# Kernel optimization log

Measured on AMD Instinct MI355X. Metric: run time of the kernel, lower is better.

The kernel has to match this reference:

```python
import jax, jax.numpy as jnp
import numpy as np

MODES_X = 16
MODES_Y = 16


def setup_inputs() -> dict:
    key = jax.random.key(0)
    ks = jax.random.split(key, 8)
    B, H, W, C = 32, 128, 128, 64
    scale = 1.0 / (C * C)
    x = jax.random.normal(ks[0], (B, H, W, C), dtype=jnp.float32)
    w1_real = scale * jax.random.normal(ks[1], (MODES_X, MODES_Y, C, C), dtype=jnp.float32)
    w1_imag = scale * jax.random.normal(ks[2], (MODES_X, MODES_Y, C, C), dtype=jnp.float32)
    w2_real = scale * jax.random.normal(ks[3], (MODES_X, MODES_Y, C, C), dtype=jnp.float32)
    w2_imag = scale * jax.random.normal(ks[4], (MODES_X, MODES_Y, C, C), dtype=jnp.float32)
    dense_kernel = jax.random.normal(ks[5], (C, C), dtype=jnp.float32) / np.sqrt(C)
    dense_bias = jnp.zeros((C,), dtype=jnp.float32)
    return {"x": x, "w1_real": w1_real, "w1_imag": w1_imag,
            "w2_real": w2_real, "w2_imag": w2_imag,
            "dense_kernel": dense_kernel, "dense_bias": dense_bias}


def _spectral_conv2d(x, w1, w2, mx, my):
    # x: [B,H,W,C] real; w1,w2: [mx,my,C,C] complex
    B, H, W, C = x.shape
    x_ft = jnp.fft.rfft2(x, axes=(1, 2))  # [B,H,W//2+1,C] complex64
    out_ft = jnp.zeros((B, H, W // 2 + 1, C), dtype=x_ft.dtype)
    # low positive x-frequencies
    out_ft = out_ft.at[:, :mx, :my].set(
        jnp.einsum('bxyi,xyio->bxyo', x_ft[:, :mx, :my], w1))
    # low negative x-frequencies
    out_ft = out_ft.at[:, -mx:, :my].set(
        jnp.einsum('bxyi,xyio->bxyo', x_ft[:, -mx:, :my], w2))
    return jnp.fft.irfft2(out_ft, s=(H, W), axes=(1, 2))


def reference(x, w1_real, w1_imag, w2_real, w2_imag, dense_kernel, dense_bias):
    w1 = w1_real + 1j * w1_imag
    w2 = w2_real + 1j * w2_imag
    y_s = _spectral_conv2d(x, w1, w2, MODES_X, MODES_Y)
    y_p = jnp.einsum('bhwi,io->bhwo', x, dense_kernel) + dense_bias
    return jax.nn.gelu(x + y_s + y_p, approximate=True)
```

## Files before the change

### kernel.cpp

```cpp
#include <hip/hip_runtime.h>
#include <math.h>

#define BB 32
#define HH 128
#define WW 128
#define CC 64
#define MX 16
#define MY 16
#define NKX 32

#define TWOPI 6.283185307179586f

typedef __attribute__((ext_vector_type(8))) short bf16x8;
typedef __attribute__((ext_vector_type(4))) float f32x4;

__device__ inline unsigned short f2bf(float f) {
    union { float f; unsigned u; } v; v.f = f;
    unsigned r = v.u + 0x7FFFu + ((v.u >> 16) & 1u);
    return (unsigned short)(r >> 16);
}


__global__ __launch_bounds__(256) void kT(const float* __restrict__ K, unsigned short* __restrict__ FR) {
    __shared__ float2 tw[128];
    int tid = threadIdx.x;
    if (tid < 128) {
        float s, c;
        sincosf(TWOPI * (float)tid * (1.0f / 128.0f), &s, &c);
        tw[tid] = make_float2(c, s);
    }
    __syncthreads();
    int g = blockIdx.x * 256 + tid;
    short v[8];
    if (g < 512) {
        int s = g;
        int l = s & 63, ks = (s >> 6) & 3, mt = s >> 8;
        int q = l >> 4, r = l & 15;
        int row = mt * 16 + r, ky = row >> 1, ri = row & 1;
        int k0 = ks * 32 + q * 8;
        #pragma unroll
        for (int e = 0; e < 8; ++e) {
            float2 t = tw[(ky * (k0 + e)) & 127];
            v[e] = (short)f2bf(ri ? -t.y : t.x);
        }
    } else if (g < 2560) {
        int s = g - 512;
        int l = s & 63, ks = (s >> 6) & 7, mt = s >> 9;
        int q = l >> 4, r = l & 15;
        int row = mt * 16 + r, kxi = row >> 1, rr = row & 1;
        int kx = (kxi < 16) ? kxi : (96 + kxi);
        int k0 = ks * 32 + q * 8;
        #pragma unroll
        for (int e = 0; e < 8; ++e) {
            int k = k0 + e, h = k >> 1, ri = k & 1;
            float2 t = tw[(kx * h) & 127];
            float val = (rr == 0) ? (ri == 0 ? t.x : t.y) : (ri == 0 ? -t.y : t.x);
            v[e] = (short)f2bf(val);
        }
    } else if (g < 3584) {
        int s = g - 2560;
        int l = s & 63, ks = (s >> 6) & 1, mt = s >> 7;
        int q = l >> 4, r = l & 15;
        int h = mt * 16 + r;
        int k0 = ks * 32 + q * 8;
        #pragma unroll
        for (int e = 0; e < 8; ++e) {
            int k = k0 + e, kxi = k >> 1, ri = k & 1;
            int kx = (kxi < 16) ? kxi : (96 + kxi);
            float2 t = tw[(kx * h) & 127];
            v[e] = (short)f2bf(ri == 0 ? t.x : -t.y);
        }
    } else if (g < 4096) {
        int s = g - 3584;
        int l = s & 63, tm = s >> 6;
        int q = l >> 4, r = l & 15;
        int row = tm * 16 + r;
        const float inv = 1.0f / 16384.0f;
        #pragma unroll
        for (int e = 0; e < 8; ++e) {
            int ky = 4 * q + (e >> 1);
            float sc = ((ky == 0) ? 1.0f : 2.0f) * inv;
            float2 t = tw[(ky * row) & 127];
            v[e] = (short)f2bf((e & 1) ? (-t.y * sc) : (t.x * sc));
        }
    } else {
        int s = g - 4096;
        int l = s & 63, ks = (s >> 6) & 1, nt = s >> 7;
        int q = l >> 4, r = l & 15;
        int col = nt * 16 + r;
        #pragma unroll
        for (int e = 0; e < 8; ++e) {
            int k = ks * 32 + q * 8 + e;
            v[e] = (short)f2bf(K[k * CC + col]);
        }
    }
    *(bf16x8*)&FR[(size_t)g * 8] = *(const bf16x8*)v;
}

__global__ __launch_bounds__(256) void kA(const float* __restrict__ x, const unsigned short* __restrict__ FR,
                                          unsigned short* __restrict__ X1) {
    int tid = threadIdx.x, bh = blockIdx.x;
    int lane = tid & 63, nt = tid >> 6, q = lane >> 4, r = lane & 15;
    const float* xp = x + (size_t)bh * (WW * CC);
    bf16x8 bf[4];
    #pragma unroll
    for (int ks = 0; ks < 4; ++ks) {
        short v[8];
        #pragma unroll
        for (int e = 0; e < 8; ++e)
            v[e] = (short)f2bf(xp[(ks * 32 + q * 8 + e) * CC + nt * 16 + r]);
        bf[ks] = *(const bf16x8*)v;
    }
    f32x4 acc0 = {0.f, 0.f, 0.f, 0.f}, acc1 = {0.f, 0.f, 0.f, 0.f};
    #pragma unroll
    for (int ks = 0; ks < 4; ++ks) {
        bf16x8 a0 = *(const bf16x8*)&FR[((size_t)((0 * 4 + ks) * 64 + lane)) * 8];
        bf16x8 a1 = *(const bf16x8*)&FR[((size_t)((1 * 4 + ks) * 64 + lane)) * 8];
        acc0 = __builtin_amdgcn_mfma_f32_16x16x32_bf16(a0, bf[ks], acc0, 0, 0, 0);
        acc1 = __builtin_amdgcn_mfma_f32_16x16x32_bf16(a1, bf[ks], acc1, 0, 0, 0);
    }
    int b = bh >> 7, h = bh & 127;
    int c = nt * 16 + r;
    #pragma unroll
    for (int j = 0; j < 4; ++j) {
        int m0 = q * 4 + j;
        X1[(((size_t)b * 16 + (m0 >> 1)) * 128 + h) * 128 + (m0 & 1) * 64 + c] = f2bf(acc0[j]);
        int m1 = 16 + m0;
        X1[(((size_t)b * 16 + (m1 >> 1)) * 128 + h) * 128 + (m1 & 1) * 64 + c] = f2bf(acc1[j]);
    }
}

__global__ __launch_bounds__(256) void kB(const unsigned short* __restrict__ X1, const unsigned short* __restrict__ FR,
                                          unsigned short* __restrict__ X2) {
    int tid = threadIdx.x, blk = blockIdx.x;
    int b = blk >> 4, ky = blk & 15;
    const unsigned short* FB = FR + 4096;
    const unsigned short* p = X1 + ((size_t)b * 16 + ky) * 16384;
    int lane = tid & 63, wid = tid >> 6, q = lane >> 4, r = lane & 15;
    int col = wid * 16 + r;
    bf16x8 bf[8];
    #pragma unroll
    for (int ks = 0; ks < 8; ++ks) {
        short v[8];
        #pragma unroll
        for (int e = 0; e < 8; ++e)
            v[e] = (short)p[(ks * 32 + q * 8 + e) * 64 + col];
        bf[ks] = *(const bf16x8*)v;
    }
    #pragma unroll
    for (int mt = 0; mt < 4; ++mt) {
        f32x4 acc = {0.f, 0.f, 0.f, 0.f};
        #pragma unroll
        for (int ks = 0; ks < 8; ++ks) {
            bf16x8 a = *(const bf16x8*)&FB[((size_t)((mt * 8 + ks) * 64 + lane)) * 8];
            acc = __builtin_amdgcn_mfma_f32_16x16x32_bf16(a, bf[ks], acc, 0, 0, 0);
        }
        #pragma unroll
        for (int j = 0; j < 4; ++j) {
            int m = mt * 16 + q * 4 + j;
            int kxi = m >> 1, rr = m & 1;
            X2[(((size_t)b * NKX + kxi) * 16 + ky) * 128 + 2 * col + rr] = f2bf(acc[j]);
        }
    }
}

__global__ __launch_bounds__(256) void kC(const float* __restrict__ w1r, const float* __restrict__ w1i,
                                          const float* __restrict__ w2r, const float* __restrict__ w2i,
                                          const unsigned short* __restrict__ X2, unsigned short* __restrict__ G) {
    __shared__ float wsr[CC * CC];
    __shared__ float wsi[CC * CC];
    int tid = threadIdx.x;
    int blk = blockIdx.x;
    int kxi = blk >> 4, ky = blk & 15;
    const float* wr = (kxi < 16) ? w1r : w2r;
    const float* wi = (kxi < 16) ? w1i : w2i;
    int wx = (kxi < 16) ? kxi : (kxi - 16);
    size_t woff = ((size_t)wx * MY + ky) * (CC * CC);
    for (int i = tid * 4; i < CC * CC; i += 1024) {
        *(float4*)&wsr[i] = *(const float4*)&wr[woff + i];
        *(float4*)&wsi[i] = *(const float4*)&wi[woff + i];
    }
    __syncthreads();

    int lane = tid & 63, wid = tid >> 6;
    int q = lane >> 4, r = lane & 15;
    bf16x8 af[2][4];
    #pragma unroll
    for (int mt = 0; mt < 2; ++mt) {
        int b = mt * 16 + r;
        #pragma unroll
        for (int ks = 0; ks < 4; ++ks)
            af[mt][ks] = *(const bf16x8*)&X2[(((size_t)b * NKX + kxi) * 16 + ky) * 128 + ks * 32 + q * 8];
    }
    bf16x8 bfr[2][4];
    #pragma unroll
    for (int t = 0; t < 2; ++t) {
        int n = (wid * 2 + t) * 16 + r;
        int o = n >> 1, ro = n & 1;
        #pragma unroll
        for (int ks = 0; ks < 4; ++ks) {
            short v[8];
            #pragma unroll
            for (int e = 0; e < 8; ++e) {
                int k = ks * 32 + q * 8 + e;
                int i = k >> 1, ri = k & 1;
                float val = (ri == 0) ? (ro ? wsi[i * 64 + o] : wsr[i * 64 + o])
                                      : (ro ? wsr[i * 64 + o] : -wsi[i * 64 + o]);
                v[e] = (short)f2bf(val);
            }
            bfr[t][ks] = *(const bf16x8*)v;
        }
    }
    f32x4 acc[2][2] = {{{0.f,0.f,0.f,0.f},{0.f,0.f,0.f,0.f}},{{0.f,0.f,0.f,0.f},{0.f,0.f,0.f,0.f}}};
    #pragma unroll
    for (int ks = 0; ks < 4; ++ks)
        #pragma unroll
        for (int mt = 0; mt < 2; ++mt)
            #pragma unroll
            for (int t = 0; t < 2; ++t)
                acc[mt][t] = __builtin_amdgcn_mfma_f32_16x16x32_bf16(af[mt][ks], bfr[t][ks], acc[mt][t], 0, 0, 0);
    #pragma unroll
    for (int mt = 0; mt < 2; ++mt)
        #pragma unroll
        for (int t = 0; t < 2; ++t)
            #pragma unroll
            for (int j = 0; j < 4; ++j) {
                int b = mt * 16 + q * 4 + j;
                int n = (wid * 2 + t) * 16 + r;
                G[(((size_t)b * NKX + kxi) * 16 + ky) * 128 + n] = f2bf(acc[mt][t][j]);
            }
}

__global__ __launch_bounds__(256) void kD(const unsigned short* __restrict__ G, const unsigned short* __restrict__ FR,
                                          unsigned short* __restrict__ Zf) {
    int tid = threadIdx.x, blk = blockIdx.x;
    int b = blk >> 5, ky = (blk >> 1) & 15, mh = blk & 1;
    int lane = tid & 63, wid = tid >> 6, q = lane >> 4, r = lane & 15;
    const unsigned short* FD = FR + 20480;
    bf16x8 bfr[2][2];
    #pragma unroll
    for (int t = 0; t < 2; ++t) {
        int n = (wid * 2 + t) * 16 + r;
        #pragma unroll
        for (int ks = 0; ks < 2; ++ks) {
            short v[8];
            #pragma unroll
            for (int e = 0; e < 8; ++e) {
                int k = ks * 32 + q * 8 + e;
                int kxi = k >> 1, ri = k & 1;
                unsigned short raw = G[(((size_t)b * NKX + kxi) * 16 + ky) * 128 + (n ^ ri)];
                if (ri & (n & 1)) raw ^= 0x8000u;
                v[e] = (short)raw;
            }
            bfr[t][ks] = *(const bf16x8*)v;
        }
    }
    #pragma unroll
    for (int mt2 = 0; mt2 < 4; ++mt2) {
        int mt = mh * 4 + mt2;
        f32x4 acc[2] = {{0.f,0.f,0.f,0.f},{0.f,0.f,0.f,0.f}};
        #pragma unroll
        for (int ks = 0; ks < 2; ++ks) {
            bf16x8 a = *(const bf16x8*)&FD[((size_t)((mt * 2 + ks) * 64 + lane)) * 8];
            #pragma unroll
            for (int t = 0; t < 2; ++t)
                acc[t] = __builtin_amdgcn_mfma_f32_16x16x32_bf16(a, bfr[t][ks], acc[t], 0, 0, 0);
        }
        #pragma unroll
        for (int t = 0; t < 2; ++t)
            #pragma unroll
            for (int j = 0; j < 4; ++j) {
                int h = mt * 16 + q * 4 + j;
                int n = (wid * 2 + t) * 16 + r;
                int c = n >> 1, reim = n & 1;
                int kp = 2 * ky + reim, q2 = kp >> 3, e2 = kp & 7;
                int nt2 = c >> 4, r2 = c & 15;
                Zf[(((size_t)b * 128 + h) * 4 + nt2) * 512 + (q2 * 16 + r2) * 8 + e2] = f2bf(acc[t][j]);
            }
    }
}

__global__ __launch_bounds__(256) void kE(const float* __restrict__ x, const unsigned short* __restrict__ Zf,
                                          const unsigned short* __restrict__ FR,
                                          const float* __restrict__ bias, float* __restrict__ out) {
    __shared__ float xs[WW * 68];
    int tid = threadIdx.x, bh = blockIdx.x;
    const float* xp = x + (size_t)bh * (WW * CC);
    for (int i = tid * 4; i < WW * CC; i += 1024) {
        int w = i >> 6, c = i & 63;
        *(float4*)&xs[w * 68 + c] = *(const float4*)&xp[i];
    }
    __syncthreads();
    int lane = tid & 63, wv = tid >> 6, q = lane >> 4, r = lane & 15;
    const unsigned short* FEAT = FR + 28672;
    const unsigned short* FEBK = FR + 32768;
    bf16x8 ax[2][2], at[2];
    #pragma unroll
    for (int t2 = 0; t2 < 2; ++t2) {
        int tm = wv * 2 + t2;
        int row = tm * 16 + r;
        #pragma unroll
        for (int ks = 0; ks < 2; ++ks) {
            const float* s = &xs[row * 68 + ks * 32 + q * 8];
            short v[8];
            #pragma unroll
            for (int e = 0; e < 8; ++e) v[e] = (short)f2bf(s[e]);
            ax[t2][ks] = *(const bf16x8*)v;
        }
        at[t2] = *(const bf16x8*)&FEAT[((size_t)(tm * 64 + lane)) * 8];
    }
    #pragma unroll
    for (int nt = 0; nt < 4; ++nt) {
        bf16x8 b0 = *(const bf16x8*)&FEBK[((size_t)((nt * 2 + 0) * 64 + lane)) * 8];
        bf16x8 b1 = *(const bf16x8*)&FEBK[((size_t)((nt * 2 + 1) * 64 + lane)) * 8];
        bf16x8 bz = *(const bf16x8*)&Zf[((size_t)bh * 4 + nt) * 512 + lane * 8];
        int c = nt * 16 + r;
        float bsv = bias[c];
        #pragma unroll
        for (int t2 = 0; t2 < 2; ++t2) {
            int tm = wv * 2 + t2;
            f32x4 acc = {0.f, 0.f, 0.f, 0.f};
            acc = __builtin_amdgcn_mfma_f32_16x16x32_bf16(ax[t2][0], b0, acc, 0, 0, 0);
            acc = __builtin_amdgcn_mfma_f32_16x16x32_bf16(ax[t2][1], b1, acc, 0, 0, 0);
            acc = __builtin_amdgcn_mfma_f32_16x16x32_bf16(at[t2], bz, acc, 0, 0, 0);
            #pragma unroll
            for (int j = 0; j < 4; ++j) {
                int w = tm * 16 + q * 4 + j;
                float u = acc[j] + xs[w * 68 + c] + bsv;
                float t = u + 0.044715f * u * u * u;
                float e = __expf(-1.5957691216057308f * t);
                out[(size_t)bh * (WW * CC) + w * CC + c] = u / (1.0f + e);
            }
        }
    }
}

extern "C" void kernel_launch(void* const* d_in, const int* in_sizes, int n_in,
                              void* d_out, int out_size, void* d_ws, size_t ws_size,
                              hipStream_t stream) {
    const float* x   = (const float*)d_in[0];
    const float* w1r = (const float*)d_in[1];
    const float* w1i = (const float*)d_in[2];
    const float* w2r = (const float*)d_in[3];
    const float* w2i = (const float*)d_in[4];
    const float* dk  = (const float*)d_in[5];
    const float* db  = (const float*)d_in[6];
    float* out = (float*)d_out;

    unsigned short* FR = (unsigned short*)d_ws;
    unsigned short* X1 = FR + 65536;
    unsigned short* X2 = X1 + 8388608;
    unsigned short* G  = X2 + 2097152;
    unsigned short* Zf = G  + 2097152;

    kT<<<18, 256, 0, stream>>>(dk, FR);
    kA<<<BB * HH, 256, 0, stream>>>(x, FR, X1);
    kB<<<BB * MY, 256, 0, stream>>>(X1, FR, X2);
    kC<<<NKX * MY, 256, 0, stream>>>(w1r, w1i, w2r, w2i, X2, G);
    kD<<<BB * MY * 2, 256, 0, stream>>>(G, FR, Zf);
    kE<<<BB * HH, 256, 0, stream>>>(x, Zf, FR, db, out);
}
```

Baseline: 321.2 us.

## Stage global loads and stores through shared memory for coalesced access in kA-kD

Each of kernels kA, kB, kC and kD now loads its input tile into shared memory with vectorized, coalesced reads before building MFMA fragments. Where a kernel scatters its output, it first writes to a shared-memory tile and then stores to global memory in 16-byte vectors. kC also converts the weights to bf16 while staging them, which halves its LDS footprint. The aim is to remove strided, element-wise global accesses, at the cost of extra barriers and more LDS use, which may lower occupancy.

```diff
diff --git a/kernel.cpp b/kernel.cpp
--- a/kernel.cpp
+++ b/kernel.cpp
@@ -99,76 +99,106 @@
 
 __global__ __launch_bounds__(256) void kA(const float* __restrict__ x, const unsigned short* __restrict__ FR,
                                           unsigned short* __restrict__ X1) {
+    __shared__ unsigned short xbf[WW * CC];
     int tid = threadIdx.x, bh = blockIdx.x;
+    const float* xp = x + (size_t)bh * (WW * CC);
+    for (int i = tid * 4; i < WW * CC; i += 1024) {
+        float4 v = *(const float4*)&xp[i];
+        ushort4 pk = make_ushort4(f2bf(v.x), f2bf(v.y), f2bf(v.z), f2bf(v.w));
+        *(ushort4*)&xbf[i] = pk;
+    }
+    __syncthreads();
     int lane = tid & 63, nt = tid >> 6, q = lane >> 4, r = lane & 15;
-    const float* xp = x + (size_t)bh * (WW * CC);
-    bf16x8 bf[4];
+    bf16x8 bfv[4];
     #pragma unroll
     for (int ks = 0; ks < 4; ++ks) {
         short v[8];
         #pragma unroll
         for (int e = 0; e < 8; ++e)
-            v[e] = (short)f2bf(xp[(ks * 32 + q * 8 + e) * CC + nt * 16 + r]);
-        bf[ks] = *(const bf16x8*)v;
+            v[e] = (short)xbf[(ks * 32 + q * 8 + e) * CC + nt * 16 + r];
+        bfv[ks] = *(const bf16x8*)v;
     }
     f32x4 acc0 = {0.f, 0.f, 0.f, 0.f}, acc1 = {0.f, 0.f, 0.f, 0.f};
     #pragma unroll
     for (int ks = 0; ks < 4; ++ks) {
         bf16x8 a0 = *(const bf16x8*)&FR[((size_t)((0 * 4 + ks) * 64 + lane)) * 8];
         bf16x8 a1 = *(const bf16x8*)&FR[((size_t)((1 * 4 + ks) * 64 + lane)) * 8];
-        acc0 = __builtin_amdgcn_mfma_f32_16x16x32_bf16(a0, bf[ks], acc0, 0, 0, 0);
-        acc1 = __builtin_amdgcn_mfma_f32_16x16x32_bf16(a1, bf[ks], acc1, 0, 0, 0);
-    }
-    int b = bh >> 7, h = bh & 127;
+        acc0 = __builtin_amdgcn_mfma_f32_16x16x32_bf16(a0, bfv[ks], acc0, 0, 0, 0);
+        acc1 = __builtin_amdgcn_mfma_f32_16x16x32_bf16(a1, bfv[ks], acc1, 0, 0, 0);
+    }
+    __syncthreads();
+    unsigned short* asT = xbf;
     int c = nt * 16 + r;
     #pragma unroll
     for (int j = 0; j < 4; ++j) {
         int m0 = q * 4 + j;
-        X1[(((size_t)b * 16 + (m0 >> 1)) * 128 + h) * 128 + (m0 & 1) * 64 + c] = f2bf(acc0[j]);
-        int m1 = 16 + m0;
-        X1[(((size_t)b * 16 + (m1 >> 1)) * 128 + h) * 128 + (m1 & 1) * 64 + c] = f2bf(acc1[j]);
-    }
+        asT[m0 * 64 + c] = f2bf(acc0[j]);
+        asT[(16 + m0) * 64 + c] = f2bf(acc1[j]);
+    }
+    __syncthreads();
+    int b = bh >> 7, h = bh & 127;
+    int ky = tid >> 4, idx8 = tid & 15;
+    int ri = idx8 >> 3, c0 = (idx8 & 7) * 8;
+    bf16x8 vv = *(const bf16x8*)&asT[(2 * ky + ri) * 64 + c0];
+    *(bf16x8*)&X1[(((size_t)b * 16 + ky) * 128 + h) * 128 + ri * 64 + c0] = vv;
 }
 
 __global__ __launch_bounds__(256) void kB(const unsigned short* __restrict__ X1, const unsigned short* __restrict__ FR,
                                           unsigned short* __restrict__ X2) {
+    __shared__ unsigned short xb[256 * 64];
     int tid = threadIdx.x, blk = blockIdx.x;
     int b = blk >> 4, ky = blk & 15;
+    const unsigned short* p = X1 + ((size_t)b * 16 + ky) * 16384;
+    for (int i = tid * 8; i < 256 * 64; i += 2048)
+        *(bf16x8*)&xb[i] = *(const bf16x8*)&p[i];
+    __syncthreads();
     const unsigned short* FB = FR + 4096;
-    const unsigned short* p = X1 + ((size_t)b * 16 + ky) * 16384;
     int lane = tid & 63, wid = tid >> 6, q = lane >> 4, r = lane & 15;
     int col = wid * 16 + r;
-    bf16x8 bf[8];
+    bf16x8 bfv[8];
     #pragma unroll
     for (int ks = 0; ks < 8; ++ks) {
         short v[8];
         #pragma unroll
         for (int e = 0; e < 8; ++e)
-            v[e] = (short)p[(ks * 32 + q * 8 + e) * 64 + col];
-        bf[ks] = *(const bf16x8*)v;
-    }
-    #pragma unroll
-    for (int mt = 0; mt < 4; ++mt) {
-        f32x4 acc = {0.f, 0.f, 0.f, 0.f};
-        #pragma unroll
-        for (int ks = 0; ks < 8; ++ks) {
+            v[e] = (short)xb[(ks * 32 + q * 8 + e) * 64 + col];
+        bfv[ks] = *(const bf16x8*)v;
+    }
+    f32x4 acc[4] = {{0.f,0.f,0.f,0.f},{0.f,0.f,0.f,0.f},{0.f,0.f,0.f,0.f},{0.f,0.f,0.f,0.f}};
+    #pragma unroll
+    for (int ks = 0; ks < 8; ++ks) {
+        #pragma unroll
+        for (int mt = 0; mt < 4; ++mt) {
             bf16x8 a = *(const bf16x8*)&FB[((size_t)((mt * 8 + ks) * 64 + lane)) * 8];
-            acc = __builtin_amdgcn_mfma_f32_16x16x32_bf16(a, bf[ks], acc, 0, 0, 0);
-        }
-        #pragma unroll
-        for (int j = 0; j < 4; ++j) {
-            int m = mt * 16 + q * 4 + j;
-            int kxi = m >> 1, rr = m & 1;
-            X2[(((size_t)b * NKX + kxi) * 16 + ky) * 128 + 2 * col + rr] = f2bf(acc[j]);
-        }
-    }
+            acc[mt] = __builtin_amdgcn_mfma_f32_16x16x32_bf16(a, bfv[ks], acc[mt], 0, 0, 0);
+        }
+    }
+    __syncthreads();
+    unsigned short* asT = xb;
+    #pragma unroll
+    for (int mt = 0; mt < 4; ++mt)
+        #pragma unroll
+        for (int j = 0; j < 4; ++j)
+            asT[(mt * 16 + q * 4 + j) * 64 + col] = f2bf(acc[mt][j]);
+    __syncthreads();
+    int kxi = tid >> 3, part = tid & 7;
+    short v2[16];
+    #pragma unroll
+    for (int s = 0; s < 16; ++s) {
+        int n = part * 16 + s, cc2 = n >> 1, rr = n & 1;
+        v2[s] = (short)asT[(2 * kxi + rr) * 64 + cc2];
+    }
+    unsigned short* dst = &X2[(((size_t)b * NKX + kxi) * 16 + ky) * 128 + part * 16];
+    *(bf16x8*)&dst[0] = *(const bf16x8*)&v2[0];
+    *(bf16x8*)&dst[8] = *(const bf16x8*)&v2[8];
 }
 
 __global__ __launch_bounds__(256) void kC(const float* __restrict__ w1r, const float* __restrict__ w1i,
                                           const float* __restrict__ w2r, const float* __restrict__ w2i,
                                           const unsigned short* __restrict__ X2, unsigned short* __restrict__ G) {
-    __shared__ float wsr[CC * CC];
-    __shared__ float wsi[CC * CC];
+    __shared__ unsigned short wbr[CC * CC];
+    __shared__ unsigned short wbi[CC * CC];
+    __shared__ unsigned short asT[32 * 128];
     int tid = threadIdx.x;
     int blk = blockIdx.x;
     int kxi = blk >> 4, ky = blk & 15;
@@ -177,8 +207,10 @@
     int wx = (kxi < 16) ? kxi : (kxi - 16);
     size_t woff = ((size_t)wx * MY + ky) * (CC * CC);
     for (int i = tid * 4; i < CC * CC; i += 1024) {
-        *(float4*)&wsr[i] = *(const float4*)&wr[woff + i];
-        *(float4*)&wsi[i] = *(const float4*)&wi[woff + i];
+        float4 a = *(const float4*)&wr[woff + i];
+        float4 bq = *(const float4*)&wi[woff + i];
+        *(ushort4*)&wbr[i] = make_ushort4(f2bf(a.x), f2bf(a.y), f2bf(a.z), f2bf(a.w));
+        *(ushort4*)&wbi[i] = make_ushort4(f2bf(bq.x), f2bf(bq.y), f2bf(bq.z), f2bf(bq.w));
     }
     __syncthreads();
 
@@ -204,9 +236,9 @@
             for (int e = 0; e < 8; ++e) {
                 int k = ks * 32 + q * 8 + e;
                 int i = k >> 1, ri = k & 1;
-                float val = (ri == 0) ? (ro ? wsi[i * 64 + o] : wsr[i * 64 + o])
-                                      : (ro ? wsr[i * 64 + o] : -wsi[i * 64 + o]);
-                v[e] = (short)f2bf(val);
+                unsigned short raw = (ri == 0) ? (ro ? wbi[i * 64 + o] : wbr[i * 64 + o])
+                                               : (ro ? wbr[i * 64 + o] : (unsigned short)(wbi[i * 64 + o] ^ 0x8000u));
+                v[e] = (short)raw;
             }
             bfr[t][ks] = *(const bf16x8*)v;
         }
@@ -224,17 +256,27 @@
         #pragma unroll
         for (int t = 0; t < 2; ++t)
             #pragma unroll
-            for (int j = 0; j < 4; ++j) {
-                int b = mt * 16 + q * 4 + j;
-                int n = (wid * 2 + t) * 16 + r;
-                G[(((size_t)b * NKX + kxi) * 16 + ky) * 128 + n] = f2bf(acc[mt][t][j]);
-            }
+            for (int j = 0; j < 4; ++j)
+                asT[(mt * 16 + q * 4 + j) * 128 + (wid * 2 + t) * 16 + r] = f2bf(acc[mt][t][j]);
+    __syncthreads();
+    int bb = tid >> 3, part = tid & 7;
+    bf16x8 u0 = *(const bf16x8*)&asT[bb * 128 + part * 16];
+    bf16x8 u1 = *(const bf16x8*)&asT[bb * 128 + part * 16 + 8];
+    unsigned short* dst = &G[(((size_t)bb * NKX + kxi) * 16 + ky) * 128 + part * 16];
+    *(bf16x8*)&dst[0] = u0;
+    *(bf16x8*)&dst[8] = u1;
 }
 
 __global__ __launch_bounds__(256) void kD(const unsigned short* __restrict__ G, const unsigned short* __restrict__ FR,
                                           unsigned short* __restrict__ Zf) {
+    __shared__ unsigned short gs[NKX * 128];
     int tid = threadIdx.x, blk = blockIdx.x;
     int b = blk >> 5, ky = (blk >> 1) & 15, mh = blk & 1;
+    for (int i = tid * 8; i < NKX * 128; i += 2048) {
+        int kxi = i >> 7, n = i & 127;
+        *(bf16x8*)&gs[i] = *(const bf16x8*)&G[(((size_t)b * NKX + kxi) * 16 + ky) * 128 + n];
+    }
+    __syncthreads();
     int lane = tid & 63, wid = tid >> 6, q = lane >> 4, r = lane & 15;
     const unsigned short* FD = FR + 20480;
     bf16x8 bfr[2][2];
@@ -248,7 +290,7 @@
             for (int e = 0; e < 8; ++e) {
                 int k = ks * 32 + q * 8 + e;
                 int kxi = k >> 1, ri = k & 1;
-                unsigned short raw = G[(((size_t)b * NKX + kxi) * 16 + ky) * 128 + (n ^ ri)];
+                unsigned short raw = gs[kxi * 128 + (n ^ ri)];
                 if (ri & (n & 1)) raw ^= 0x8000u;
                 v[e] = (short)raw;
             }
```

After: 328.4 us. 2.2% more time.
